# Performance work log

Hardware: AMD Instinct MI355X
Metric: run time of the kernel (lower is better)

## Reference

```python
import jax, jax.numpy as jnp
import numpy as np

N = 100000
E = 3200000
F_IN = 128
H = 16
NUM_GRAPHS = 1000


def gcn_conv(x, W, b, src, dst, norm, n_nodes):
    # x: [N, Fin] -> h: [N, Fout]; gather along src, scale, scatter-add to dst
    h = x @ W
    msg = h[src] * norm[:, None]            # [E_tot, Fout]
    out = jax.ops.segment_sum(msg, dst, num_segments=n_nodes)
    return out + b


def setup_inputs() -> dict:
    key = jax.random.key(0)
    k0, k1, k2, k3, k4, k5 = jax.random.split(key, 6)
    x = jax.random.normal(k0, (N, F_IN), dtype=jnp.float32)
    edge_index = jax.random.randint(k1, (2, E), 0, N, dtype=jnp.int64)
    batch = jnp.sort(jax.random.randint(k2, (N,), 0, NUM_GRAPHS, dtype=jnp.int64))
    # Glorot-style init for GCN weights, zero bias (PyG default)
    W1 = jax.random.normal(k3, (F_IN, H), dtype=jnp.float32) / np.sqrt(F_IN)
    b1 = jnp.zeros((H,), dtype=jnp.float32)
    W2 = jax.random.normal(k4, (H, 1), dtype=jnp.float32) / np.sqrt(H)
    b2 = jnp.zeros((1,), dtype=jnp.float32)
    return {"x": x, "edge_index": edge_index, "batch": batch,
            "W1": W1, "b1": b1, "W2": W2, "b2": b2}


def reference(x, edge_index, batch, W1, b1, W2, b2):
    n_nodes = x.shape[0]
    # add self-loops (PyG GCNConv default)
    loop = jnp.arange(n_nodes, dtype=edge_index.dtype)
    src = jnp.concatenate([edge_index[0], loop])
    dst = jnp.concatenate([edge_index[1], loop])
    # symmetric normalization D^{-1/2} (A+I) D^{-1/2}
    deg = jax.ops.segment_sum(jnp.ones_like(dst, dtype=x.dtype), dst,
                              num_segments=n_nodes)
    dinv = jnp.where(deg > 0, jax.lax.rsqrt(deg), 0.0)
    norm = dinv[src] * dinv[dst]            # [E_tot]

    h = gcn_conv(x, W1, b1, src, dst, norm, n_nodes)   # [N, 16]
    h = jax.nn.relu(h)
    h = gcn_conv(h, W2, b2, src, dst, norm, n_nodes)   # [N, 1]
    # global_add_pool over graphs
    out = jax.ops.segment_sum(h, batch, num_segments=NUM_GRAPHS)  # [G, 1]
    return out
```

## Files before the change

### kernel.cpp

```cpp
#include <hip/hip_runtime.h>

#define NB_MAX   512
#define CHUNK    8192
#define CAPB     16384
#define SORT_CAP 12288

__device__ inline unsigned short f2bf(float f) {
    unsigned u = __float_as_uint(f);
    u += 0x7FFFu + ((u >> 16) & 1u);
    return (unsigned short)(u >> 16);
}

__global__ void k_zero(float* __restrict__ out, int g, int* __restrict__ bcnt) {
    int t = blockIdx.x * blockDim.x + threadIdx.x;
    if (t < g) out[t] = 0.f;
    if (t < NB_MAX) bcnt[t] = 0;
}

__global__ __launch_bounds__(512) void k_scatter(const int* __restrict__ src,
                                                 const int* __restrict__ dst,
                                                 int* __restrict__ bcnt,
                                                 int* __restrict__ packed,
                                                 int E) {
    __shared__ int lh[NB_MAX];
    __shared__ int lscan[NB_MAX];
    __shared__ int ldelta[NB_MAX];
    __shared__ int sorted[CHUNK];
    __shared__ unsigned short sbkt[CHUNK];
    int t = threadIdx.x;
    int e0 = blockIdx.x * CHUNK;
    int e1 = min(e0 + CHUNK, E);
    int cnt = e1 - e0;
    lh[t] = 0;
    __syncthreads();
    for (int e = e0 + t; e < e1; e += 512) atomicAdd(&lh[dst[e] >> 8], 1);
    __syncthreads();
    int v = lh[t];
    lscan[t] = v;
    __syncthreads();
    for (int o = 1; o < 512; o <<= 1) {
        int u = (t >= o) ? lscan[t - o] : 0;
        __syncthreads();
        lscan[t] += u;
        __syncthreads();
    }
    int ex = lscan[t] - v;
    int gbase = v ? atomicAdd(&bcnt[t], v) : 0;
    lh[t] = ex;
    ldelta[t] = t * CAPB + gbase - ex;
    __syncthreads();
    for (int e = e0 + t; e < e1; e += 512) {
        int d = dst[e];
        int b = d >> 8;
        int r = atomicAdd(&lh[b], 1);
        sorted[r] = src[e] | ((d & 255) << 24);
        sbkt[r] = (unsigned short)b;
    }
    __syncthreads();
    for (int i = t; i < cnt; i += 512)
        packed[i + ldelta[sbkt[i]]] = sorted[i];
}

__global__ __launch_bounds__(512) void k_sort2(const int* __restrict__ packed,
                                               const int* __restrict__ bcnt,
                                               int* __restrict__ sidx2,
                                               int* __restrict__ noffs,
                                               int* __restrict__ ndeg,
                                               float* __restrict__ dinv, int n) {
    __shared__ int hist[256];
    __shared__ int scan[256];
    __shared__ int curs[256];
    __shared__ int sorted[SORT_CAP];
    int t = threadIdx.x, b = blockIdx.x;
    int seg0 = b * CAPB, cnt = bcnt[b];
    if (t < 256) hist[t] = 0;
    __syncthreads();
    for (int e = t; e < cnt; e += 512)
        atomicAdd(&hist[(unsigned)packed[seg0 + e] >> 24], 1);
    __syncthreads();
    int v = 0;
    if (t < 256) { v = hist[t]; scan[t] = v; }
    __syncthreads();
    for (int o = 1; o < 256; o <<= 1) {
        int u = (t < 256 && t >= o) ? scan[t - o] : 0;
        __syncthreads();
        if (t < 256) scan[t] += u;
        __syncthreads();
    }
    int ex = 0;
    if (t < 256) {
        ex = scan[t] - v;
        int node = (b << 8) + t;
        if (node < n) {
            noffs[node] = seg0 + ex;
            ndeg[node] = v;
            dinv[node] = rsqrtf((float)v + 1.0f);
        }
    }
    if (cnt <= SORT_CAP) {
        if (t < 256) curs[t] = ex;
        __syncthreads();
        for (int e = t; e < cnt; e += 512) {
            int p = packed[seg0 + e];
            int dl = (int)((unsigned)p >> 24);
            int r = atomicAdd(&curs[dl], 1);
            sorted[r] = p & 0xFFFFFF;
        }
        __syncthreads();
        for (int i = t; i < cnt; i += 512)
            sidx2[seg0 + i] = sorted[i];
    } else {
        if (t < 256) curs[t] = seg0 + ex;
        __syncthreads();
        for (int e = t; e < cnt; e += 512) {
            int p = packed[seg0 + e];
            int dl = (int)((unsigned)p >> 24);
            int r = atomicAdd(&curs[dl], 1);
            sidx2[r] = p & 0xFFFFFF;
        }
    }
}

__global__ __launch_bounds__(256) void k_gemm1(const float* __restrict__ x,
                                               const float* __restrict__ W1,
                                               const float* __restrict__ dinv,
                                               unsigned short* __restrict__ hs, int n) {
    __shared__ float sW[128 * 16];
    __shared__ float sXT[32 * 260];
    int t = threadIdx.x;
    for (int q = t; q < 2048; q += 256) sW[q] = W1[q];
    int node0 = blockIdx.x * 256;
    int ng = t >> 2, cg = t & 3;
    int sub = t & 7, rbase = t >> 3;
    float acc[4][4];
#pragma unroll
    for (int i = 0; i < 4; i++)
#pragma unroll
        for (int j = 0; j < 4; j++) acc[i][j] = 0.f;
    for (int kc = 0; kc < 4; kc++) {
        __syncthreads();
#pragma unroll
        for (int pass = 0; pass < 8; pass++) {
            int row = pass * 32 + rbase;
            int node = node0 + row;
            const float* xp = x + (size_t)min(node, n - 1) * 128 + kc * 32 + sub * 4;
            float4 v = *(const float4*)xp;
            int k0 = sub * 4;
            sXT[(k0 + 0) * 260 + row] = v.x;
            sXT[(k0 + 1) * 260 + row] = v.y;
            sXT[(k0 + 2) * 260 + row] = v.z;
            sXT[(k0 + 3) * 260 + row] = v.w;
        }
        __syncthreads();
        const float* wbase = sW + kc * 32 * 16 + cg * 4;
#pragma unroll 8
        for (int k = 0; k < 32; k++) {
            float4 xv = *(const float4*)&sXT[k * 260 + ng * 4];
            float4 wv = *(const float4*)&wbase[k * 16];
            acc[0][0] += xv.x * wv.x; acc[0][1] += xv.x * wv.y;
            acc[0][2] += xv.x * wv.z; acc[0][3] += xv.x * wv.w;
            acc[1][0] += xv.y * wv.x; acc[1][1] += xv.y * wv.y;
            acc[1][2] += xv.y * wv.z; acc[1][3] += xv.y * wv.w;
            acc[2][0] += xv.z * wv.x; acc[2][1] += xv.z * wv.y;
            acc[2][2] += xv.z * wv.z; acc[2][3] += xv.z * wv.w;
            acc[3][0] += xv.w * wv.x; acc[3][1] += xv.w * wv.y;
            acc[3][2] += xv.w * wv.z; acc[3][3] += xv.w * wv.w;
        }
    }
#pragma unroll
    for (int i = 0; i < 4; i++) {
        int node = node0 + ng * 4 + i;
        if (node < n) {
            float di = dinv[node];
            ushort4 o;
            o.x = f2bf(acc[i][0] * di);
            o.y = f2bf(acc[i][1] * di);
            o.z = f2bf(acc[i][2] * di);
            o.w = f2bf(acc[i][3] * di);
            *(ushort4*)&hs[(size_t)node * 16 + cg * 4] = o;
        }
    }
}

#define UNPACK_ADD(u)                                        \
    acc[0] += __uint_as_float((u).x << 16);                  \
    acc[1] += __uint_as_float((u).x & 0xFFFF0000u);          \
    acc[2] += __uint_as_float((u).y << 16);                  \
    acc[3] += __uint_as_float((u).y & 0xFFFF0000u);          \
    acc[4] += __uint_as_float((u).z << 16);                  \
    acc[5] += __uint_as_float((u).z & 0xFFFF0000u);          \
    acc[6] += __uint_as_float((u).w << 16);                  \
    acc[7] += __uint_as_float((u).w & 0xFFFF0000u);

__global__ __launch_bounds__(256) void k_agg1(const uint4* __restrict__ hs4,
                                              const int* __restrict__ noffs,
                                              const int* __restrict__ ndeg,
                                              const int* __restrict__ sidx2,
                                              const float* __restrict__ dinv,
                                              const float* __restrict__ b1,
                                              const float* __restrict__ W2,
                                              float* __restrict__ hw, int n) {
    int tid = blockIdx.x * 256 + threadIdx.x;
    int node = tid >> 1, q = tid & 1;
    if (node >= n) return;
    float acc[8];
    uint4 u0 = hs4[(size_t)node * 2 + q];
    acc[0] = __uint_as_float(u0.x << 16);
    acc[1] = __uint_as_float(u0.x & 0xFFFF0000u);
    acc[2] = __uint_as_float(u0.y << 16);
    acc[3] = __uint_as_float(u0.y & 0xFFFF0000u);
    acc[4] = __uint_as_float(u0.z << 16);
    acc[5] = __uint_as_float(u0.z & 0xFFFF0000u);
    acc[6] = __uint_as_float(u0.w << 16);
    acc[7] = __uint_as_float(u0.w & 0xFFFF0000u);
    int e0 = noffs[node], e1 = e0 + ndeg[node];
    int e = e0;
    for (; e + 3 < e1; e += 4) {
        int s0 = sidx2[e], s1 = sidx2[e + 1];
        int s2 = sidx2[e + 2], s3 = sidx2[e + 3];
        uint4 a = hs4[(size_t)s0 * 2 + q];
        uint4 c = hs4[(size_t)s1 * 2 + q];
        uint4 d = hs4[(size_t)s2 * 2 + q];
        uint4 f = hs4[(size_t)s3 * 2 + q];
        UNPACK_ADD(a) UNPACK_ADD(c) UNPACK_ADD(d) UNPACK_ADD(f)
    }
    for (; e < e1; e++) {
        uint4 a = hs4[(size_t)sidx2[e] * 2 + q];
        UNPACK_ADD(a)
    }
    float di = dinv[node];
    int base = q * 8;
    float r = 0.f;
#pragma unroll
    for (int j = 0; j < 8; j++)
        r += fmaxf(di * acc[j] + b1[base + j], 0.f) * W2[base + j];
    r += __shfl_down(r, 1, 2);
    if (q == 0) hw[node] = r * di;
}

__global__ __launch_bounds__(256) void k_agg2(const float* __restrict__ hw,
                                              const int* __restrict__ noffs,
                                              const int* __restrict__ ndeg,
                                              const int* __restrict__ sidx2,
                                              const float* __restrict__ dinv,
                                              const float* __restrict__ b2,
                                              const int* __restrict__ batch,
                                              float* __restrict__ out, int n) {
    __shared__ float v[256];
    __shared__ int g[256];
    int t = threadIdx.x;
    int i = blockIdx.x * 256 + t;
    float val = 0.f;
    int gid = -1;
    if (i < n) {
        float acc = hw[i];
        int e0 = noffs[i], e1 = e0 + ndeg[i];
        int e = e0;
        for (; e + 1 < e1; e += 2) {
            float a = hw[sidx2[e]];
            float c = hw[sidx2[e + 1]];
            acc += a + c;
        }
        if (e < e1) acc += hw[sidx2[e]];
        val = dinv[i] * acc + b2[0];
        gid = batch[i];
    }
    v[t] = val;
    g[t] = gid;
    __syncthreads();
    if (gid >= 0 && (t == 0 || g[t - 1] != gid)) {
        float s = val;
        for (int q = t + 1; q < 256 && g[q] == gid; q++) s += v[q];
        atomicAdd(&out[gid], s);
    }
}

extern "C" void kernel_launch(void* const* d_in, const int* in_sizes, int n_in,
                              void* d_out, int out_size, void* d_ws, size_t ws_size,
                              hipStream_t stream) {
    int n = in_sizes[0] / 128;
    int E = in_sizes[1] / 2;
    const float* x     = (const float*)d_in[0];
    const int*   ei    = (const int*)d_in[1];
    const int*   src   = ei;
    const int*   dst   = ei + E;
    const int*   batch = (const int*)d_in[2];
    const float* W1    = (const float*)d_in[3];
    const float* b1    = (const float*)d_in[4];
    const float* W2    = (const float*)d_in[5];
    const float* b2    = (const float*)d_in[6];
    float* out = (float*)d_out;

    int nb = (n + 255) >> 8;

    char* p = (char*)d_ws;
    auto carve = [&](size_t bytes) {
        void* r = (void*)p;
        p += (bytes + 63) & ~(size_t)63;
        return r;
    };
    int*            bcnt   = (int*)carve(NB_MAX * 4);
    int*            packed = (int*)carve((size_t)nb * CAPB * 4);
    int*            sidx2  = (int*)carve((size_t)nb * CAPB * 4);
    int*            noffs  = (int*)carve((size_t)n * 4);
    int*            ndeg   = (int*)carve((size_t)n * 4);
    float*          dinv   = (float*)carve((size_t)n * 4);
    unsigned short* hs     = (unsigned short*)carve((size_t)n * 16 * 2);
    float*          hw     = (float*)carve((size_t)n * 4);

    k_zero<<<(out_size + 1023) / 1024, 1024, 0, stream>>>(out, out_size, bcnt);
    k_scatter<<<(E + CHUNK - 1) / CHUNK, 512, 0, stream>>>(src, dst, bcnt, packed, E);
    k_sort2<<<nb, 512, 0, stream>>>(packed, bcnt, sidx2, noffs, ndeg, dinv, n);
    k_gemm1<<<nb, 256, 0, stream>>>(x, W1, dinv, hs, n);
    k_agg1<<<((size_t)n * 2 + 255) / 256, 256, 0, stream>>>((const uint4*)hs, noffs, ndeg,
                                                            sidx2, dinv, b1, W2, hw, n);
    k_agg2<<<nb, 256, 0, stream>>>(hw, noffs, ndeg, sidx2, dinv, b2, batch, out, n);
}
```

Measured before the change: 132.8 us.

## Fuse bucket sort with first GEMM, deepen agg1 unroll, split agg2 edges over two lanes

Merges the per-bucket counting sort and the x@W1 GEMM into one kernel, reusing the sort's shared buffer for the transposed x tile and keeping dinv in shared memory. This saves a launch and a global dinv reload. k_agg1 now issues eight neighbor gathers per iteration instead of four to expose more memory-level parallelism. k_agg2 splits each node's edge list across two lanes and combines them with a shuffle. The fused kernel leaves half its threads idle during the GEMM and uses more shared memory per block, which may reduce occupancy.

```diff
diff --git a/kernel.cpp b/kernel.cpp
--- a/kernel.cpp
+++ b/kernel.cpp
@@ -61,18 +61,30 @@
         packed[i + ldelta[sbkt[i]]] = sorted[i];
 }
 
-__global__ __launch_bounds__(512) void k_sort2(const int* __restrict__ packed,
-                                               const int* __restrict__ bcnt,
-                                               int* __restrict__ sidx2,
-                                               int* __restrict__ noffs,
-                                               int* __restrict__ ndeg,
-                                               float* __restrict__ dinv, int n) {
+__global__ __launch_bounds__(512) void k_sortgemm(const int* __restrict__ packed,
+                                                  const int* __restrict__ bcnt,
+                                                  const float* __restrict__ x,
+                                                  const float* __restrict__ W1,
+                                                  int* __restrict__ sidx2,
+                                                  int* __restrict__ noffs,
+                                                  int* __restrict__ ndeg,
+                                                  float* __restrict__ dinv,
+                                                  unsigned short* __restrict__ hs,
+                                                  int n) {
     __shared__ int hist[256];
     __shared__ int scan[256];
     __shared__ int curs[256];
-    __shared__ int sorted[SORT_CAP];
+    __shared__ float sdinv[256];
+    __shared__ float sW[128 * 16];
+    __shared__ __align__(16) char smem[SORT_CAP * 4];
+    int* sorted = (int*)smem;
+    float* sXT = (float*)smem;
+
     int t = threadIdx.x, b = blockIdx.x;
     int seg0 = b * CAPB, cnt = bcnt[b];
+    int node0 = b << 8;
+
+    for (int q = t; q < 2048; q += 512) sW[q] = W1[q];
     if (t < 256) hist[t] = 0;
     __syncthreads();
     for (int e = t; e < cnt; e += 512)
@@ -90,11 +102,13 @@
     int ex = 0;
     if (t < 256) {
         ex = scan[t] - v;
-        int node = (b << 8) + t;
+        float di = rsqrtf((float)v + 1.0f);
+        sdinv[t] = di;
+        int node = node0 + t;
         if (node < n) {
             noffs[node] = seg0 + ex;
             ndeg[node] = v;
-            dinv[node] = rsqrtf((float)v + 1.0f);
+            dinv[node] = di;
         }
     }
     if (cnt <= SORT_CAP) {
@@ -119,19 +133,8 @@
             sidx2[r] = p & 0xFFFFFF;
         }
     }
-}
-
-__global__ __launch_bounds__(256) void k_gemm1(const float* __restrict__ x,
-                                               const float* __restrict__ W1,
-                                               const float* __restrict__ dinv,
-                                               unsigned short* __restrict__ hs, int n) {
-    __shared__ float sW[128 * 16];
-    __shared__ float sXT[32 * 260];
-    int t = threadIdx.x;
-    for (int q = t; q < 2048; q += 256) sW[q] = W1[q];
-    int node0 = blockIdx.x * 256;
+
     int ng = t >> 2, cg = t & 3;
-    int sub = t & 7, rbase = t >> 3;
     float acc[4][4];
 #pragma unroll
     for (int i = 0; i < 4; i++)
@@ -140,44 +143,49 @@
     for (int kc = 0; kc < 4; kc++) {
         __syncthreads();
 #pragma unroll
-        for (int pass = 0; pass < 8; pass++) {
-            int row = pass * 32 + rbase;
+        for (int pass = 0; pass < 4; pass++) {
+            int row = pass * 64 + (t >> 3);
             int node = node0 + row;
-            const float* xp = x + (size_t)min(node, n - 1) * 128 + kc * 32 + sub * 4;
-            float4 v = *(const float4*)xp;
-            int k0 = sub * 4;
-            sXT[(k0 + 0) * 260 + row] = v.x;
-            sXT[(k0 + 1) * 260 + row] = v.y;
-            sXT[(k0 + 2) * 260 + row] = v.z;
-            sXT[(k0 + 3) * 260 + row] = v.w;
-        }
-        __syncthreads();
-        const float* wbase = sW + kc * 32 * 16 + cg * 4;
+            const float* xp = x + (size_t)min(node, n - 1) * 128 + kc * 32 + (t & 7) * 4;
+            float4 vv = *(const float4*)xp;
+            int k0 = (t & 7) * 4;
+            sXT[(k0 + 0) * 260 + row] = vv.x;
+            sXT[(k0 + 1) * 260 + row] = vv.y;
+            sXT[(k0 + 2) * 260 + row] = vv.z;
+            sXT[(k0 + 3) * 260 + row] = vv.w;
+        }
+        __syncthreads();
+        if (t < 256) {
+            const float* wbase = sW + kc * 32 * 16 + cg * 4;
 #pragma unroll 8
-        for (int k = 0; k < 32; k++) {
-            float4 xv = *(const float4*)&sXT[k * 260 + ng * 4];
-            float4 wv = *(const float4*)&wbase[k * 16];
-            acc[0][0] += xv.x * wv.x; acc[0][1] += xv.x * wv.y;
-            acc[0][2] += xv.x * wv.z; acc[0][3] += xv.x * wv.w;
-            acc[1][0] += xv.y * wv.x; acc[1][1] += xv.y * wv.y;
-            acc[1][2] += xv.y * wv.z; acc[1][3] += xv.y * wv.w;
-            acc[2][0] += xv.z * wv.x; acc[2][1] += xv.z * wv.y;
-            acc[2][2] += xv.z * wv.z; acc[2][3] += xv.z * wv.w;
-            acc[3][0] += xv.w * wv.x; acc[3][1] += xv.w * wv.y;
-            acc[3][2] += xv.w * wv.z; acc[3][3] += xv.w * wv.w;
-        }
-    }
-#pragma unroll
-    for (int i = 0; i < 4; i++) {
-        int node = node0 + ng * 4 + i;
-        if (node < n) {
-            float di = dinv[node];
-            ushort4 o;
-            o.x = f2bf(acc[i][0] * di);
-            o.y = f2bf(acc[i][1] * di);
-            o.z = f2bf(acc[i][2] * di);
-            o.w = f2bf(acc[i][3] * di);
-            *(ushort4*)&hs[(size_t)node * 16 + cg * 4] = o;
+            for (int k = 0; k < 32; k++) {
+                float4 xv = *(const float4*)&sXT[k * 260 + ng * 4];
+                float4 wv = *(const float4*)&wbase[k * 16];
+                acc[0][0] += xv.x * wv.x; acc[0][1] += xv.x * wv.y;
+                acc[0][2] += xv.x * wv.z; acc[0][3] += xv.x * wv.w;
+                acc[1][0] += xv.y * wv.x; acc[1][1] += xv.y * wv.y;
+                acc[1][2] += xv.y * wv.z; acc[1][3] += xv.y * wv.w;
+                acc[2][0] += xv.z * wv.x; acc[2][1] += xv.z * wv.y;
+                acc[2][2] += xv.z * wv.z; acc[2][3] += xv.z * wv.w;
+                acc[3][0] += xv.w * wv.x; acc[3][1] += xv.w * wv.y;
+                acc[3][2] += xv.w * wv.z; acc[3][3] += xv.w * wv.w;
+            }
+        }
+    }
+    if (t < 256) {
+#pragma unroll
+        for (int i = 0; i < 4; i++) {
+            int local = ng * 4 + i;
+            int node = node0 + local;
+            if (node < n) {
+                float di = sdinv[local];
+                ushort4 o;
+                o.x = f2bf(acc[i][0] * di);
+                o.y = f2bf(acc[i][1] * di);
+                o.z = f2bf(acc[i][2] * di);
+                o.w = f2bf(acc[i][3] * di);
+                *(ushort4*)&hs[(size_t)node * 16 + cg * 4] = o;
+            }
         }
     }
 }
@@ -215,14 +223,21 @@
     acc[7] = __uint_as_float(u0.w & 0xFFFF0000u);
     int e0 = noffs[node], e1 = e0 + ndeg[node];
     int e = e0;
-    for (; e + 3 < e1; e += 4) {
-        int s0 = sidx2[e], s1 = sidx2[e + 1];
+    for (; e + 7 < e1; e += 8) {
+        int s0 = sidx2[e],     s1 = sidx2[e + 1];
         int s2 = sidx2[e + 2], s3 = sidx2[e + 3];
-        uint4 a = hs4[(size_t)s0 * 2 + q];
-        uint4 c = hs4[(size_t)s1 * 2 + q];
-        uint4 d = hs4[(size_t)s2 * 2 + q];
-        uint4 f = hs4[(size_t)s3 * 2 + q];
-        UNPACK_ADD(a) UNPACK_ADD(c) UNPACK_ADD(d) UNPACK_ADD(f)
+        int s4 = sidx2[e + 4], s5 = sidx2[e + 5];
+        int s6 = sidx2[e + 6], s7 = sidx2[e + 7];
+        uint4 a0 = hs4[(size_t)s0 * 2 + q];
+        uint4 a1 = hs4[(size_t)s1 * 2 + q];
+        uint4 a2 = hs4[(size_t)s2 * 2 + q];
+        uint4 a3 = hs4[(size_t)s3 * 2 + q];
+        uint4 a4 = hs4[(size_t)s4 * 2 + q];
+        uint4 a5 = hs4[(size_t)s5 * 2 + q];
+        uint4 a6 = hs4[(size_t)s6 * 2 + q];
+        uint4 a7 = hs4[(size_t)s7 * 2 + q];
+        UNPACK_ADD(a0) UNPACK_ADD(a1) UNPACK_ADD(a2) UNPACK_ADD(a3)
+        UNPACK_ADD(a4) UNPACK_ADD(a5) UNPACK_ADD(a6) UNPACK_ADD(a7)
     }
     for (; e < e1; e++) {
         uint4 a = hs4[(size_t)sidx2[e] * 2 + q];
@@ -246,32 +261,38 @@
                                               const float* __restrict__ b2,
                                               const int* __restrict__ batch,
                                               float* __restrict__ out, int n) {
-    __shared__ float v[256];
-    __shared__ int g[256];
+    __shared__ float v[128];
+    __shared__ int g[128];
     int t = threadIdx.x;
-    int i = blockIdx.x * 256 + t;
-    float val = 0.f;
+    int tid = blockIdx.x * 256 + t;
+    int i = tid >> 1, q = tid & 1;
+    int li = t >> 1;
+    float acc = 0.f;
     int gid = -1;
     if (i < n) {
-        float acc = hw[i];
+        if (q == 0) acc = hw[i];
         int e0 = noffs[i], e1 = e0 + ndeg[i];
-        int e = e0;
-        for (; e + 1 < e1; e += 2) {
-            float a = hw[sidx2[e]];
-            float c = hw[sidx2[e + 1]];
-            acc += a + c;
-        }
-        if (e < e1) acc += hw[sidx2[e]];
-        val = dinv[i] * acc + b2[0];
-        gid = batch[i];
-    }
-    v[t] = val;
-    g[t] = gid;
-    __syncthreads();
-    if (gid >= 0 && (t == 0 || g[t - 1] != gid)) {
-        float s = val;
-        for (int q = t + 1; q < 256 && g[q] == gid; q++) s += v[q];
-        atomicAdd(&out[gid], s);
+        int e = e0 + q;
+        for (; e + 6 < e1; e += 8)
+            acc += hw[sidx2[e]] + hw[sidx2[e + 2]] + hw[sidx2[e + 4]] + hw[sidx2[e + 6]];
+        for (; e < e1; e += 2) acc += hw[sidx2[e]];
+    }
+    acc += __shfl_down(acc, 1, 2);
+    if (i < n && q == 0) {
+        v[li] = dinv[i] * acc + b2[0];
+        g[li] = batch[i];
+    } else if (q == 0) {
+        v[li] = 0.f;
+        g[li] = -1;
+    }
+    __syncthreads();
+    if (q == 0) {
+        int gid2 = g[li];
+        if (gid2 >= 0 && (li == 0 || g[li - 1] != gid2)) {
+            float s = v[li];
+            for (int w = li + 1; w < 128 && g[w] == gid2; w++) s += v[w];
+            atomicAdd(&out[gid2], s);
+        }
     }
 }
 
@@ -310,9 +331,10 @@
 
     k_zero<<<(out_size + 1023) / 1024, 1024, 0, stream>>>(out, out_size, bcnt);
     k_scatter<<<(E + CHUNK - 1) / CHUNK, 512, 0, stream>>>(src, dst, bcnt, packed, E);
-    k_sort2<<<nb, 512, 0, stream>>>(packed, bcnt, sidx2, noffs, ndeg, dinv, n);
-    k_gemm1<<<nb, 256, 0, stream>>>(x, W1, dinv, hs, n);
+    k_sortgemm<<<nb, 512, 0, stream>>>(packed, bcnt, x, W1, sidx2, noffs, ndeg,
+                                       dinv, hs, n);
     k_agg1<<<((size_t)n * 2 + 255) / 256, 256, 0, stream>>>((const uint4*)hs, noffs, ndeg,
                                                             sidx2, dinv, b1, W2, hw, n);
-    k_agg2<<<nb, 256, 0, stream>>>(hw, noffs, ndeg, sidx2, dinv, b2, batch, out, n);
-}
+    k_agg2<<<((size_t)n * 2 + 255) / 256, 256, 0, stream>>>(hw, noffs, ndeg, sidx2,
+                                                            dinv, b2, batch, out, n);
+}
```

Result: faster. 120.9 us (-8.9%).
